# Kernel tuning notes

Measured on AMD Instinct MI355X. Metric: run time of the kernel, lower is better.

## Reference

```python
import jax, jax.numpy as jnp
import numpy as np

D_MODEL = 1024
NUM_HEADS = 16
DEPTH = D_MODEL // NUM_HEADS
B, S = 4, 1024


def setup_inputs() -> dict:
    key = jax.random.key(0)
    ks = jax.random.split(key, 9)
    scale = 0.02
    return {
        "v": jax.random.normal(ks[0], (B, S, D_MODEL), jnp.float32),
        "k": jax.random.normal(ks[1], (B, S, D_MODEL), jnp.float32),
        "q": jax.random.normal(ks[2], (B, S, D_MODEL), jnp.float32),
        "wq_w": jax.random.normal(ks[3], (D_MODEL, D_MODEL), jnp.float32) * scale,
        "wq_b": jax.random.normal(ks[4], (D_MODEL,), jnp.float32) * scale,
        "wv_w": jax.random.normal(ks[5], (D_MODEL, D_MODEL), jnp.float32) * scale,
        "wv_b": jax.random.normal(ks[6], (D_MODEL,), jnp.float32) * scale,
        "dense_w": jax.random.normal(ks[7], (D_MODEL, D_MODEL), jnp.float32) * scale,
        "dense_b": jax.random.normal(ks[8], (D_MODEL,), jnp.float32) * scale,
    }


def _split_heads(x):
    # [B, S, D] -> [B, H, S, depth]
    b, s, _ = x.shape
    return x.reshape(b, s, NUM_HEADS, DEPTH).transpose(0, 2, 1, 3)


def reference(v, k, q, wq_w, wq_b, wv_w, wv_b, dense_w, dense_b):
    # Faithful to original torch module, including its bugs:
    #   v = wv(v); k = wv(v)  (k input and wk layer unused)
    #   output = logits @ v   (raw logits, NOT softmax weights)
    del k  # unused in original forward (overwritten)
    q_p = q @ wq_w.T + wq_b
    v_p = v @ wv_w.T + wv_b
    k_p = v_p @ wv_w.T + wv_b  # k = self.wv(v) after v already projected

    qh = _split_heads(q_p)  # [B,H,S,dh]
    kh = _split_heads(k_p)
    vh = _split_heads(v_p)

    logits = jnp.einsum("bhsd,bhtd->bhst", qh, kh) / jnp.sqrt(
        jnp.asarray(DEPTH, jnp.float32)
    )  # [B,H,S,S]
    attention_weights = jax.nn.softmax(logits, axis=-1)
    # BUG preserved: uses logits, not attention_weights
    attn_out = jnp.einsum("bhst,bhtd->bhsd", logits, vh)  # [B,H,S,dh]

    concat = attn_out.transpose(0, 2, 1, 3).reshape(B, S, D_MODEL)
    output = concat @ dense_w.T + dense_b
    # dropout is identity in eval mode
    return output, attention_weights
```

## Files before the change

kernel.cpp:

```cpp
#include <hip/hip_runtime.h>
#include <hip/hip_bf16.h>

#define DM 1024
#define BS 4
#define SS 1024
#define NH 16

typedef __attribute__((ext_vector_type(8))) short bf16x8;
typedef __attribute__((ext_vector_type(4))) float f32x4;

__device__ inline unsigned short f2bf(float x) {
    union { float f; unsigned u; } v; v.f = x;
    unsigned r = v.u + 0x7fffu + ((v.u >> 16) & 1u);
    return (unsigned short)(r >> 16);
}

template<typename T> __device__ inline void store1(T* p, float v);
template<> __device__ inline void store1<float>(float* p, float v) { *p = v; }
template<> __device__ inline void store1<unsigned short>(unsigned short* p, float v) { *p = f2bf(v); }

__device__ inline void glds16(const unsigned short* g, unsigned short* l) {
    __builtin_amdgcn_global_load_lds(
        (const __attribute__((address_space(1))) unsigned int*)g,
        (__attribute__((address_space(3))) unsigned int*)l, 16, 0, 0);
}

__global__ __launch_bounds__(256) void cvt_bf16(const float* __restrict__ in,
                                                unsigned short* __restrict__ out, int n4)
{
    int i = blockIdx.x * blockDim.x + threadIdx.x;
    const int stride = gridDim.x * blockDim.x;
    for (; i < n4; i += stride) {
        float4 v = reinterpret_cast<const float4*>(in)[i];
        ushort4 o;
        o.x = f2bf(v.x); o.y = f2bf(v.y); o.z = f2bf(v.z); o.w = f2bf(v.w);
        reinterpret_cast<ushort4*>(out)[i] = o;
    }
}

template<typename TO>
__global__ __launch_bounds__(256) void gemm64_bt(
    const unsigned short* __restrict__ A, int lda,
    const unsigned short* __restrict__ B, int ldb,
    TO* __restrict__ C, int ldc,
    const float* __restrict__ bias, int K, float scale)
{
    __shared__ unsigned short lA[64 * 32];
    __shared__ unsigned short lB[64 * 32];

    const int tid = threadIdx.x;
    const int wid = tid >> 6, lane = tid & 63;
    const int wr = wid >> 1, wc = wid & 1;
    const int r0 = lane & 15;
    const int kq = (lane >> 4) * 8;
    const int srow = lane >> 2;
    const int scol = (lane & 3) * 8;

    const unsigned short* Ap = A + (long long)blockIdx.y * 64 * lda;
    const unsigned short* Bp = B + (long long)blockIdx.x * 64 * ldb;
    TO* Cp = C + (long long)blockIdx.y * 64 * ldc + blockIdx.x * 64;

    f32x4 acc[2][2];
    #pragma unroll
    for (int m = 0; m < 2; ++m)
        #pragma unroll
        for (int n = 0; n < 2; ++n)
            acc[m][n] = f32x4{0.f, 0.f, 0.f, 0.f};

    for (int kt = 0; kt < K; kt += 32) {
        __syncthreads();
        glds16(Ap + (long long)(wid * 16 + srow) * lda + kt + scol, &lA[wid * 512]);
        glds16(Bp + (long long)(wid * 16 + srow) * ldb + kt + scol, &lB[wid * 512]);
        __syncthreads();

        bf16x8 af[2], bfr[2];
        #pragma unroll
        for (int m = 0; m < 2; ++m)
            af[m] = *reinterpret_cast<const bf16x8*>(&lA[(wr * 32 + m * 16 + r0) * 32 + kq]);
        #pragma unroll
        for (int n = 0; n < 2; ++n)
            bfr[n] = *reinterpret_cast<const bf16x8*>(&lB[(wc * 32 + n * 16 + r0) * 32 + kq]);
        #pragma unroll
        for (int m = 0; m < 2; ++m)
            #pragma unroll
            for (int n = 0; n < 2; ++n)
                acc[m][n] = __builtin_amdgcn_mfma_f32_16x16x32_bf16(af[m], bfr[n], acc[m][n], 0, 0, 0);
    }

    const int cf = lane & 15, rf = (lane >> 4) * 4;
    #pragma unroll
    for (int m = 0; m < 2; ++m) {
        #pragma unroll
        for (int n = 0; n < 2; ++n) {
            int col = wc * 32 + n * 16 + cf;
            float bv = bias ? bias[blockIdx.x * 64 + col] : 0.0f;
            #pragma unroll
            for (int j = 0; j < 4; ++j) {
                int row = wr * 32 + m * 16 + rf + j;
                store1<TO>(&Cp[(long long)row * ldc + col], acc[m][n][j] * scale + bv);
            }
        }
    }
}

__global__ __launch_bounds__(256) void transpose_vh(const unsigned short* __restrict__ vp,
                                                    unsigned short* __restrict__ vT)
{
    __shared__ unsigned short tile[64][65];
    const int bh = blockIdx.y;
    const int b = bh >> 4, h = bh & 15;
    const long long t0 = (long long)blockIdx.x * 64;
    const int tid = threadIdx.x;
    #pragma unroll
    for (int kk = 0; kk < 4; ++kk) {
        int l = tid + kk * 256;
        int row = l >> 4, c4 = l & 15;
        const unsigned short* src = vp + ((long long)b * SS + t0 + row) * DM + h * 64 + c4 * 4;
        ushort4 val = *reinterpret_cast<const ushort4*>(src);
        tile[row][c4 * 4 + 0] = val.x;
        tile[row][c4 * 4 + 1] = val.y;
        tile[row][c4 * 4 + 2] = val.z;
        tile[row][c4 * 4 + 3] = val.w;
    }
    __syncthreads();
    #pragma unroll
    for (int kk = 0; kk < 4; ++kk) {
        int l = tid + kk * 256;
        int d = l >> 4, i4 = l & 15;
        ushort4 o;
        o.x = tile[i4 * 4 + 0][d];
        o.y = tile[i4 * 4 + 1][d];
        o.z = tile[i4 * 4 + 2][d];
        o.w = tile[i4 * 4 + 3][d];
        *reinterpret_cast<ushort4*>(vT + ((long long)bh * 64 + d) * SS + t0 + i4 * 4) = o;
    }
}

__global__ __launch_bounds__(256) void fused_attn2(
    const unsigned short* __restrict__ qp,
    const unsigned short* __restrict__ kp,
    const unsigned short* __restrict__ vT,
    float* __restrict__ attnw,
    unsigned short* __restrict__ cc)
{
    constexpr int LSTR = 1032;
    __shared__ alignas(16) unsigned short S16[16 * LSTR];
    __shared__ float mW[4][16];
    __shared__ float sW[4][16];
    __shared__ float rowMax[16];
    __shared__ float rowInv[16];

    const int tid = threadIdx.x;
    const int w = tid >> 6;
    const int lane = tid & 63;
    const int lg = lane >> 4;
    const int ln = lane & 15;
    const int z = blockIdx.y, b = z >> 4, h = z & 15;
    const int row0 = blockIdx.x * 16;

    const unsigned short* qbase = qp + ((long long)b * SS + row0) * DM + h * 64;
    const unsigned short* kbase = kp + (long long)b * SS * DM + h * 64;
    const unsigned short* vbase = vT + (long long)z * 64 * SS;

    bf16x8 qf[2];
    #pragma unroll
    for (int ks = 0; ks < 2; ++ks)
        qf[ks] = *reinterpret_cast<const bf16x8*>(qbase + (long long)ln * DM + ks * 32 + lg * 8);

    float sreg[8][2][4];
    #pragma unroll
    for (int c = 0; c < 8; ++c) {
        const int colbase = c * 128 + w * 32;
        f32x4 sac[2];
        sac[0] = f32x4{0.f, 0.f, 0.f, 0.f};
        sac[1] = f32x4{0.f, 0.f, 0.f, 0.f};
        #pragma unroll
        for (int ks = 0; ks < 2; ++ks) {
            #pragma unroll
            for (int cf2 = 0; cf2 < 2; ++cf2) {
                bf16x8 kf = *reinterpret_cast<const bf16x8*>(
                    kbase + (long long)(colbase + cf2 * 16 + ln) * DM + ks * 32 + lg * 8);
                sac[cf2] = __builtin_amdgcn_mfma_f32_16x16x32_bf16(qf[ks], kf, sac[cf2], 0, 0, 0);
            }
        }
        #pragma unroll
        for (int cf2 = 0; cf2 < 2; ++cf2)
            #pragma unroll
            for (int j = 0; j < 4; ++j) {
                float s = sac[cf2][j] * 0.125f;
                sreg[c][cf2][j] = s;
                S16[(lg * 4 + j) * LSTR + colbase + cf2 * 16 + ln] = f2bf(s);
            }
    }

    float m4[4];
    #pragma unroll
    for (int j = 0; j < 4; ++j) {
        float mx = sreg[0][0][j];
        #pragma unroll
        for (int c = 0; c < 8; ++c)
            #pragma unroll
            for (int cf2 = 0; cf2 < 2; ++cf2)
                mx = fmaxf(mx, sreg[c][cf2][j]);
        #pragma unroll
        for (int o = 1; o < 16; o <<= 1) mx = fmaxf(mx, __shfl_xor(mx, o));
        m4[j] = mx;
    }
    if (ln == 0) {
        #pragma unroll
        for (int j = 0; j < 4; ++j) mW[w][lg * 4 + j] = m4[j];
    }
    __syncthreads();
    if (tid < 16)
        rowMax[tid] = fmaxf(fmaxf(mW[0][tid], mW[1][tid]), fmaxf(mW[2][tid], mW[3][tid]));
    __syncthreads();
    float s4[4];
    #pragma unroll
    for (int j = 0; j < 4; ++j) {
        float mf = rowMax[lg * 4 + j];
        float se = 0.f;
        #pragma unroll
        for (int c = 0; c < 8; ++c)
            #pragma unroll
            for (int cf2 = 0; cf2 < 2; ++cf2)
                se += __expf(sreg[c][cf2][j] - mf);
        #pragma unroll
        for (int o = 1; o < 16; o <<= 1) se += __shfl_xor(se, o);
        s4[j] = se;
    }
    if (ln == 0) {
        #pragma unroll
        for (int j = 0; j < 4; ++j) sW[w][lg * 4 + j] = s4[j];
    }
    __syncthreads();
    if (tid < 16)
        rowInv[tid] = 1.0f / (sW[0][tid] + sW[1][tid] + sW[2][tid] + sW[3][tid]);
    __syncthreads();

    {
        float mf[4], inv[4];
        #pragma unroll
        for (int j = 0; j < 4; ++j) {
            mf[j] = rowMax[lg * 4 + j];
            inv[j] = rowInv[lg * 4 + j];
        }
        #pragma unroll
        for (int c = 0; c < 8; ++c) {
            const int colbase = c * 128 + w * 32;
            #pragma unroll
            for (int cf2 = 0; cf2 < 2; ++cf2)
                #pragma unroll
                for (int j = 0; j < 4; ++j)
                    attnw[((long long)z * SS + row0 + lg * 4 + j) * SS + colbase + cf2 * 16 + ln] =
                        __expf(sreg[c][cf2][j] - mf[j]) * inv[j];
        }
    }

    {
        f32x4 pvn = f32x4{0.f, 0.f, 0.f, 0.f};
        const unsigned short* vrow = vbase + (long long)(w * 16 + ln) * SS;
        for (int kk = 0; kk < 32; ++kk) {
            bf16x8 sa = *reinterpret_cast<const bf16x8*>(&S16[ln * LSTR + kk * 32 + lg * 8]);
            bf16x8 vf = *reinterpret_cast<const bf16x8*>(vrow + kk * 32 + lg * 8);
            pvn = __builtin_amdgcn_mfma_f32_16x16x32_bf16(sa, vf, pvn, 0, 0, 0);
        }
        #pragma unroll
        for (int j = 0; j < 4; ++j)
            cc[((long long)b * SS + row0 + lg * 4 + j) * DM + h * 64 + w * 16 + ln] = f2bf(pvn[j]);
    }
}

extern "C" void kernel_launch(void* const* d_in, const int* in_sizes, int n_in,
                              void* d_out, int out_size, void* d_ws, size_t ws_size,
                              hipStream_t stream) {
    (void)in_sizes; (void)n_in; (void)out_size; (void)ws_size;
    const float* v    = (const float*)d_in[0];
    const float* q    = (const float*)d_in[2];
    const float* wq_w = (const float*)d_in[3];
    const float* wq_b = (const float*)d_in[4];
    const float* wv_w = (const float*)d_in[5];
    const float* wv_b = (const float*)d_in[6];
    const float* dw   = (const float*)d_in[7];
    const float* db   = (const float*)d_in[8];

    unsigned short* q_p = (unsigned short*)d_ws;
    unsigned short* v_p = q_p + (4 << 20);
    unsigned short* k_p = v_p + (4 << 20);
    unsigned short* vT  = k_p + (4 << 20);
    unsigned short* cc  = vT  + (4 << 20);

    float* out0   = (float*)d_out;
    float* attnw  = out0 + (long long)BS * SS * DM;

    unsigned short* qb  = (unsigned short*)attnw;
    unsigned short* vb  = qb  + (4 << 20);
    unsigned short* wqb = vb  + (4 << 20);
    unsigned short* wvb = wqb + (1 << 20);
    unsigned short* dwb = q_p;

    dim3 blk(256);
    dim3 gemmGrid(DM / 64, BS * SS / 64);

    cvt_bf16<<<dim3(1024), blk, 0, stream>>>(q, qb, (BS * SS * DM) / 4);
    cvt_bf16<<<dim3(1024), blk, 0, stream>>>(v, vb, (BS * SS * DM) / 4);
    cvt_bf16<<<dim3(256),  blk, 0, stream>>>(wq_w, wqb, (DM * DM) / 4);
    cvt_bf16<<<dim3(256),  blk, 0, stream>>>(wv_w, wvb, (DM * DM) / 4);

    gemm64_bt<unsigned short><<<gemmGrid, blk, 0, stream>>>(
        qb, DM, wqb, DM, q_p, DM, wq_b, DM, 1.0f);
    gemm64_bt<unsigned short><<<gemmGrid, blk, 0, stream>>>(
        vb, DM, wvb, DM, v_p, DM, wv_b, DM, 1.0f);
    gemm64_bt<unsigned short><<<gemmGrid, blk, 0, stream>>>(
        v_p, DM, wvb, DM, k_p, DM, wv_b, DM, 1.0f);

    transpose_vh<<<dim3(16, 64), blk, 0, stream>>>(v_p, vT);

    fused_attn2<<<dim3(SS / 16, BS * NH), blk, 0, stream>>>(q_p, k_p, vT, attnw, cc);

    cvt_bf16<<<dim3(256), blk, 0, stream>>>(dw, dwb, (DM * DM) / 4);
    gemm64_bt<float><<<gemmGrid, blk, 0, stream>>>(
        cc, DM, dwb, DM, out0, DM, db, DM, 1.0f);
}
```

Before: 256.1 us.

## Double-buffer GEMM LDS tiles and use online softmax with coalesced attention-weight stores

The GEMM now double-buffers its LDS tiles: it prefetches the next K slice while computing the current one, and it needs one barrier per iteration instead of two. The attention kernel drops the large per-thread score register array in favour of an online max/sum softmax, prefetches K fragments one chunk ahead, and sets a launch-bounds occupancy hint. Attention weights are now recomputed from the bf16 scores held in LDS and written as coalesced float4 rows rather than scattered scalar stores. The aim is lower register pressure, more occupancy and better store coalescing. The cost is that softmax outputs are derived from bf16-rounded logits, which loses some precision.

```diff
diff --git a/kernel.cpp b/kernel.cpp
--- a/kernel.cpp
+++ b/kernel.cpp
@@ -13,6 +13,10 @@
     union { float f; unsigned u; } v; v.f = x;
     unsigned r = v.u + 0x7fffu + ((v.u >> 16) & 1u);
     return (unsigned short)(r >> 16);
+}
+__device__ inline float bf2f(unsigned short u) {
+    union { unsigned u; float f; } v; v.u = ((unsigned)u) << 16;
+    return v.f;
 }
 
 template<typename T> __device__ inline void store1(T* p, float v);
@@ -45,8 +49,8 @@
     TO* __restrict__ C, int ldc,
     const float* __restrict__ bias, int K, float scale)
 {
-    __shared__ unsigned short lA[64 * 32];
-    __shared__ unsigned short lB[64 * 32];
+    __shared__ unsigned short lA[2][64 * 32];
+    __shared__ unsigned short lB[2][64 * 32];
 
     const int tid = threadIdx.x;
     const int wid = tid >> 6, lane = tid & 63;
@@ -56,8 +60,8 @@
     const int srow = lane >> 2;
     const int scol = (lane & 3) * 8;
 
-    const unsigned short* Ap = A + (long long)blockIdx.y * 64 * lda;
-    const unsigned short* Bp = B + (long long)blockIdx.x * 64 * ldb;
+    const unsigned short* Ap = A + ((long long)blockIdx.y * 64 + wid * 16 + srow) * lda + scol;
+    const unsigned short* Bp = B + ((long long)blockIdx.x * 64 + wid * 16 + srow) * ldb + scol;
     TO* Cp = C + (long long)blockIdx.y * 64 * ldc + blockIdx.x * 64;
 
     f32x4 acc[2][2];
@@ -67,24 +71,31 @@
         for (int n = 0; n < 2; ++n)
             acc[m][n] = f32x4{0.f, 0.f, 0.f, 0.f};
 
-    for (int kt = 0; kt < K; kt += 32) {
-        __syncthreads();
-        glds16(Ap + (long long)(wid * 16 + srow) * lda + kt + scol, &lA[wid * 512]);
-        glds16(Bp + (long long)(wid * 16 + srow) * ldb + kt + scol, &lB[wid * 512]);
-        __syncthreads();
-
+    glds16(Ap, &lA[0][wid * 512]);
+    glds16(Bp, &lB[0][wid * 512]);
+    __syncthreads();
+
+    const int NT = K / 32;
+    int cur = 0;
+    for (int t = 0; t < NT; ++t) {
+        if (t + 1 < NT) {
+            glds16(Ap + (t + 1) * 32, &lA[cur ^ 1][wid * 512]);
+            glds16(Bp + (t + 1) * 32, &lB[cur ^ 1][wid * 512]);
+        }
         bf16x8 af[2], bfr[2];
         #pragma unroll
         for (int m = 0; m < 2; ++m)
-            af[m] = *reinterpret_cast<const bf16x8*>(&lA[(wr * 32 + m * 16 + r0) * 32 + kq]);
+            af[m] = *reinterpret_cast<const bf16x8*>(&lA[cur][(wr * 32 + m * 16 + r0) * 32 + kq]);
         #pragma unroll
         for (int n = 0; n < 2; ++n)
-            bfr[n] = *reinterpret_cast<const bf16x8*>(&lB[(wc * 32 + n * 16 + r0) * 32 + kq]);
+            bfr[n] = *reinterpret_cast<const bf16x8*>(&lB[cur][(wc * 32 + n * 16 + r0) * 32 + kq]);
         #pragma unroll
         for (int m = 0; m < 2; ++m)
             #pragma unroll
             for (int n = 0; n < 2; ++n)
                 acc[m][n] = __builtin_amdgcn_mfma_f32_16x16x32_bf16(af[m], bfr[n], acc[m][n], 0, 0, 0);
+        __syncthreads();
+        cur ^= 1;
     }
 
     const int cf = lane & 15, rf = (lane >> 4) * 4;
@@ -136,7 +147,7 @@
     }
 }
 
-__global__ __launch_bounds__(256) void fused_attn2(
+__global__ __launch_bounds__(256, 4) void fused_attn3(
     const unsigned short* __restrict__ qp,
     const unsigned short* __restrict__ kp,
     const unsigned short* __restrict__ vT,
@@ -145,10 +156,9 @@
 {
     constexpr int LSTR = 1032;
     __shared__ alignas(16) unsigned short S16[16 * LSTR];
-    __shared__ float mW[4][16];
-    __shared__ float sW[4][16];
-    __shared__ float rowMax[16];
-    __shared__ float rowInv[16];
+    __shared__ float2 msW[4][16];
+    __shared__ float rowM[16];
+    __shared__ float rowI[16];
 
     const int tid = threadIdx.x;
     const int w = tid >> 6;
@@ -167,93 +177,95 @@
     for (int ks = 0; ks < 2; ++ks)
         qf[ks] = *reinterpret_cast<const bf16x8*>(qbase + (long long)ln * DM + ks * 32 + lg * 8);
 
-    float sreg[8][2][4];
-    #pragma unroll
+    float m4[4], s4[4];
+    #pragma unroll
+    for (int j = 0; j < 4; ++j) { m4[j] = -1e30f; s4[j] = 0.f; }
+
+    bf16x8 kf_cur[4];
+    #pragma unroll
+    for (int i = 0; i < 4; ++i) {
+        const int ks = i >> 1, cf2 = i & 1;
+        kf_cur[i] = *reinterpret_cast<const bf16x8*>(
+            kbase + (long long)(w * 32 + cf2 * 16 + ln) * DM + ks * 32 + lg * 8);
+    }
     for (int c = 0; c < 8; ++c) {
-        const int colbase = c * 128 + w * 32;
+        bf16x8 kf_nxt[4];
+        if (c < 7) {
+            #pragma unroll
+            for (int i = 0; i < 4; ++i) {
+                const int ks = i >> 1, cf2 = i & 1;
+                kf_nxt[i] = *reinterpret_cast<const bf16x8*>(
+                    kbase + (long long)((c + 1) * 128 + w * 32 + cf2 * 16 + ln) * DM + ks * 32 + lg * 8);
+            }
+        }
         f32x4 sac[2];
         sac[0] = f32x4{0.f, 0.f, 0.f, 0.f};
         sac[1] = f32x4{0.f, 0.f, 0.f, 0.f};
-        #pragma unroll
-        for (int ks = 0; ks < 2; ++ks) {
-            #pragma unroll
-            for (int cf2 = 0; cf2 < 2; ++cf2) {
-                bf16x8 kf = *reinterpret_cast<const bf16x8*>(
-                    kbase + (long long)(colbase + cf2 * 16 + ln) * DM + ks * 32 + lg * 8);
-                sac[cf2] = __builtin_amdgcn_mfma_f32_16x16x32_bf16(qf[ks], kf, sac[cf2], 0, 0, 0);
+        sac[0] = __builtin_amdgcn_mfma_f32_16x16x32_bf16(qf[0], kf_cur[0], sac[0], 0, 0, 0);
+        sac[1] = __builtin_amdgcn_mfma_f32_16x16x32_bf16(qf[0], kf_cur[1], sac[1], 0, 0, 0);
+        sac[0] = __builtin_amdgcn_mfma_f32_16x16x32_bf16(qf[1], kf_cur[2], sac[0], 0, 0, 0);
+        sac[1] = __builtin_amdgcn_mfma_f32_16x16x32_bf16(qf[1], kf_cur[3], sac[1], 0, 0, 0);
+
+        const int colbase = c * 128 + w * 32;
+        #pragma unroll
+        for (int cf2 = 0; cf2 < 2; ++cf2)
+            #pragma unroll
+            for (int j = 0; j < 4; ++j) {
+                unsigned short ub = f2bf(sac[cf2][j] * 0.125f);
+                S16[(lg * 4 + j) * LSTR + colbase + cf2 * 16 + ln] = ub;
+                sac[cf2][j] = bf2f(ub);
             }
-        }
-        #pragma unroll
-        for (int cf2 = 0; cf2 < 2; ++cf2)
-            #pragma unroll
-            for (int j = 0; j < 4; ++j) {
-                float s = sac[cf2][j] * 0.125f;
-                sreg[c][cf2][j] = s;
-                S16[(lg * 4 + j) * LSTR + colbase + cf2 * 16 + ln] = f2bf(s);
-            }
-    }
-
-    float m4[4];
+        #pragma unroll
+        for (int j = 0; j < 4; ++j) {
+            float v0 = sac[0][j], v1 = sac[1][j];
+            float mn = fmaxf(m4[j], fmaxf(v0, v1));
+            s4[j] = s4[j] * __expf(m4[j] - mn) + __expf(v0 - mn) + __expf(v1 - mn);
+            m4[j] = mn;
+        }
+        if (c < 7) {
+            #pragma unroll
+            for (int i = 0; i < 4; ++i) kf_cur[i] = kf_nxt[i];
+        }
+    }
+
     #pragma unroll
     for (int j = 0; j < 4; ++j) {
-        float mx = sreg[0][0][j];
-        #pragma unroll
-        for (int c = 0; c < 8; ++c)
-            #pragma unroll
-            for (int cf2 = 0; cf2 < 2; ++cf2)
-                mx = fmaxf(mx, sreg[c][cf2][j]);
-        #pragma unroll
-        for (int o = 1; o < 16; o <<= 1) mx = fmaxf(mx, __shfl_xor(mx, o));
-        m4[j] = mx;
+        #pragma unroll
+        for (int o = 1; o < 16; o <<= 1) {
+            float mo = __shfl_xor(m4[j], o);
+            float so = __shfl_xor(s4[j], o);
+            float mn = fmaxf(m4[j], mo);
+            s4[j] = s4[j] * __expf(m4[j] - mn) + so * __expf(mo - mn);
+            m4[j] = mn;
+        }
     }
     if (ln == 0) {
         #pragma unroll
-        for (int j = 0; j < 4; ++j) mW[w][lg * 4 + j] = m4[j];
+        for (int j = 0; j < 4; ++j) msW[w][lg * 4 + j] = make_float2(m4[j], s4[j]);
     }
     __syncthreads();
-    if (tid < 16)
-        rowMax[tid] = fmaxf(fmaxf(mW[0][tid], mW[1][tid]), fmaxf(mW[2][tid], mW[3][tid]));
+    if (tid < 16) {
+        float mf = -1e30f;
+        #pragma unroll
+        for (int w2 = 0; w2 < 4; ++w2) mf = fmaxf(mf, msW[w2][tid].x);
+        float sf = 0.f;
+        #pragma unroll
+        for (int w2 = 0; w2 < 4; ++w2) sf += msW[w2][tid].y * __expf(msW[w2][tid].x - mf);
+        rowM[tid] = mf;
+        rowI[tid] = 1.0f / sf;
+    }
     __syncthreads();
-    float s4[4];
-    #pragma unroll
-    for (int j = 0; j < 4; ++j) {
-        float mf = rowMax[lg * 4 + j];
-        float se = 0.f;
-        #pragma unroll
-        for (int c = 0; c < 8; ++c)
-            #pragma unroll
-            for (int cf2 = 0; cf2 < 2; ++cf2)
-                se += __expf(sreg[c][cf2][j] - mf);
-        #pragma unroll
-        for (int o = 1; o < 16; o <<= 1) se += __shfl_xor(se, o);
-        s4[j] = se;
-    }
-    if (ln == 0) {
-        #pragma unroll
-        for (int j = 0; j < 4; ++j) sW[w][lg * 4 + j] = s4[j];
-    }
-    __syncthreads();
-    if (tid < 16)
-        rowInv[tid] = 1.0f / (sW[0][tid] + sW[1][tid] + sW[2][tid] + sW[3][tid]);
-    __syncthreads();
-
-    {
-        float mf[4], inv[4];
-        #pragma unroll
-        for (int j = 0; j < 4; ++j) {
-            mf[j] = rowMax[lg * 4 + j];
-            inv[j] = rowInv[lg * 4 + j];
-        }
-        #pragma unroll
-        for (int c = 0; c < 8; ++c) {
-            const int colbase = c * 128 + w * 32;
-            #pragma unroll
-            for (int cf2 = 0; cf2 < 2; ++cf2)
-                #pragma unroll
-                for (int j = 0; j < 4; ++j)
-                    attnw[((long long)z * SS + row0 + lg * 4 + j) * SS + colbase + cf2 * 16 + ln] =
-                        __expf(sreg[c][cf2][j] - mf[j]) * inv[j];
-        }
+
+    #pragma unroll 4
+    for (int it = 0; it < 16; ++it) {
+        float mf = rowM[it], inv = rowI[it];
+        uint2 sv = *reinterpret_cast<const uint2*>(&S16[it * LSTR + tid * 4]);
+        float4 o;
+        o.x = __expf(bf2f((unsigned short)(sv.x & 0xffffu)) - mf) * inv;
+        o.y = __expf(bf2f((unsigned short)(sv.x >> 16)) - mf) * inv;
+        o.z = __expf(bf2f((unsigned short)(sv.y & 0xffffu)) - mf) * inv;
+        o.w = __expf(bf2f((unsigned short)(sv.y >> 16)) - mf) * inv;
+        *reinterpret_cast<float4*>(attnw + ((long long)z * SS + row0 + it) * SS + tid * 4) = o;
     }
 
     {
@@ -315,7 +327,7 @@
 
     transpose_vh<<<dim3(16, 64), blk, 0, stream>>>(v_p, vT);
 
-    fused_attn2<<<dim3(SS / 16, BS * NH), blk, 0, stream>>>(q_p, k_p, vT, attnw, cc);
+    fused_attn3<<<dim3(SS / 16, BS * NH), blk, 0, stream>>>(q_p, k_p, vT, attnw, cc);
 
     cvt_bf16<<<dim3(256), blk, 0, stream>>>(dw, dwb, (DM * DM) / 4);
     gemm64_bt<float><<<gemmGrid, blk, 0, stream>>>(
```

Measured after the change: 249.3 us. -2.7%, faster.
